# Kernel optimization log

Measured on AMD Instinct MI355X. Metric: run time of the kernel, lower is better.

Reference implementation:

```python
import jax, jax.numpy as jnp
import numpy as np

HIDDEN = 2048
NUM_HEADS = 32
NUM_KV_HEADS = 4
HEAD_DIM = 128
EPS = 1e-6
ROPE_THETA = 10000.0
Q_SIZE = NUM_HEADS * HEAD_DIM      # 4096
KV_SIZE = NUM_KV_HEADS * HEAD_DIM  # 512


def setup_inputs() -> dict:
    key = jax.random.key(0)
    k1, k2, k3, k4, k5 = jax.random.split(key, 5)
    T = 2048
    hidden_states = jax.random.normal(k1, (T, HIDDEN), dtype=jnp.float32)
    positions = jnp.arange(T, dtype=jnp.int64)
    # qkv_proj weight: [q_size + 2*kv_size, hidden] (torch Linear convention)
    w_qkv = jax.random.normal(k2, (Q_SIZE + 2 * KV_SIZE, HIDDEN), dtype=jnp.float32) * (HIDDEN ** -0.5)
    # o_proj weight: [hidden, num_heads*head_dim]
    w_o = jax.random.normal(k3, (HIDDEN, Q_SIZE), dtype=jnp.float32) * (Q_SIZE ** -0.5)
    q_norm_w = jnp.ones((HEAD_DIM,), dtype=jnp.float32) + 0.1 * jax.random.normal(k4, (HEAD_DIM,), dtype=jnp.float32)
    k_norm_w = jnp.ones((HEAD_DIM,), dtype=jnp.float32) + 0.1 * jax.random.normal(k5, (HEAD_DIM,), dtype=jnp.float32)
    return {"positions": positions, "hidden_states": hidden_states,
            "w_qkv": w_qkv, "w_o": w_o, "q_norm_w": q_norm_w, "k_norm_w": k_norm_w}


def _rms_norm(x, w):
    # x: [..., head_dim]; normalize over last dim
    var = jnp.mean(jnp.square(x), axis=-1, keepdims=True)
    return x * jax.lax.rsqrt(var + EPS) * w


def _rope(positions, x):
    # neox-style rotary over full head_dim. x: [T, H, D]
    half = HEAD_DIM // 2
    inv_freq = 1.0 / (ROPE_THETA ** (jnp.arange(0, half, dtype=jnp.float32) / half))
    freqs = positions.astype(jnp.float32)[:, None] * inv_freq[None, :]  # [T, half]
    cos = jnp.cos(freqs)[:, None, :]  # [T, 1, half]
    sin = jnp.sin(freqs)[:, None, :]
    x1, x2 = x[..., :half], x[..., half:]
    return jnp.concatenate([x1 * cos - x2 * sin, x2 * cos + x1 * sin], axis=-1)


def reference(positions, hidden_states, w_qkv, w_o, q_norm_w, k_norm_w):
    T = hidden_states.shape[0]
    qkv = hidden_states @ w_qkv.T  # [T, q_size+2*kv_size]
    q, k, v = jnp.split(qkv, [Q_SIZE, Q_SIZE + KV_SIZE], axis=-1)
    q = _rms_norm(q.reshape(T, NUM_HEADS, HEAD_DIM), q_norm_w)
    k = _rms_norm(k.reshape(T, NUM_KV_HEADS, HEAD_DIM), k_norm_w)
    v = v.reshape(T, NUM_KV_HEADS, HEAD_DIM)
    q = _rope(positions, q)
    k = _rope(positions, k)
    # GQA: expand kv heads to query heads
    rep = NUM_HEADS // NUM_KV_HEADS
    k = jnp.repeat(k, rep, axis=1)  # [T, H, D]
    v = jnp.repeat(v, rep, axis=1)
    scale = HEAD_DIM ** -0.5
    scores = jnp.einsum('qhd,khd->hqk', q, k) * scale  # [H, T, T]
    causal = jnp.tril(jnp.ones((T, T), dtype=bool))
    scores = jnp.where(causal[None, :, :], scores, jnp.float32(-1e30))
    probs = jax.nn.softmax(scores, axis=-1)
    attn = jnp.einsum('hqk,khd->qhd', probs, v).reshape(T, Q_SIZE)
    return attn @ w_o.T  # [T, hidden]
```

## Files before the change

kernel.cpp:

```cpp
#include <hip/hip_runtime.h>

#define T_TOK   2048
#define HID     2048
#define NHEADS  32
#define NKV     4
#define HD      128
#define QSZ     4096
#define KVSZ    512
#define QKVW    5120

typedef unsigned short u16;
typedef __bf16 bf16x8 __attribute__((ext_vector_type(8)));
typedef float  f32x4  __attribute__((ext_vector_type(4)));

__device__ __forceinline__ u16 f2bf(float f) {
  unsigned int u = __float_as_uint(f);
  u += 0x7fffu + ((u >> 16) & 1u);
  return (u16)(u >> 16);
}

__device__ __forceinline__ void gl2lds16(const void* g, void* l) {
  __builtin_amdgcn_global_load_lds(
      (const __attribute__((address_space(1))) unsigned int*)g,
      (__attribute__((address_space(3))) unsigned int*)l, 16, 0, 0);
}

__global__ void cvt3_f32_bf16(const float* __restrict__ in0, u16* __restrict__ o0, int n0,
                              const float* __restrict__ in1, u16* __restrict__ o1, int n1,
                              const float* __restrict__ in2, u16* __restrict__ o2, int n2) {
  int i = blockIdx.x * blockDim.x + threadIdx.x;
  const float* in; u16* out;
  if (i < n0)            { in = in0; out = o0; }
  else if (i < n0 + n1)  { in = in1; out = o1; i -= n0; }
  else if (i < n0+n1+n2) { in = in2; out = o2; i -= n0 + n1; }
  else return;
  float4 v = ((const float4*)in)[i];
  ushort4 o;
  o.x = f2bf(v.x); o.y = f2bf(v.y); o.z = f2bf(v.z); o.w = f2bf(v.w);
  ((ushort4*)out)[i] = o;
}

template<int BM>
__launch_bounds__(256, 2)
__global__ void gemm_nt(const u16* __restrict__ A, const u16* __restrict__ B,
                        float* __restrict__ C, int M, int N, int K) {
  constexpr int MI = BM / 32;
  __shared__ __align__(16) u16 As[BM * 32];
  __shared__ __align__(16) u16 Bs[128 * 32];
  const int tid  = threadIdx.x;
  const int wave = tid >> 6, lane = tid & 63;
  const int l15  = lane & 15, quad = lane >> 4;
  const int wr   = wave >> 1, wc = wave & 1;

  const u16* Ab = A + (size_t)blockIdx.y * BM * K;
  const u16* Bb = B + (size_t)blockIdx.x * 128 * K;

  f32x4 acc[MI][4];
#pragma unroll
  for (int i = 0; i < MI; i++)
#pragma unroll
    for (int j = 0; j < 4; j++) acc[i][j] = (f32x4){0.f, 0.f, 0.f, 0.f};

  constexpr int ACH = BM * 32 / 8;
  for (int k0 = 0; k0 < K; k0 += 32) {
#pragma unroll
    for (int s = 0; s < (ACH + 512) / 256; s++) {
      int c = tid + s * 256;
      if (c < ACH) {
        int row = c >> 2, co = (c & 3) * 8;
        gl2lds16(Ab + (size_t)row * K + k0 + co, &As[c * 8]);
      } else {
        int c2 = c - ACH;
        int row = c2 >> 2, co = (c2 & 3) * 8;
        gl2lds16(Bb + (size_t)row * K + k0 + co, &Bs[c2 * 8]);
      }
    }
    __syncthreads();
    bf16x8 af[MI], bf[4];
#pragma unroll
    for (int i = 0; i < MI; i++) af[i] = *(const bf16x8*)&As[(wr * (BM / 2) + i * 16 + l15) * 32 + quad * 8];
#pragma unroll
    for (int j = 0; j < 4; j++) bf[j] = *(const bf16x8*)&Bs[(wc * 64 + j * 16 + l15) * 32 + quad * 8];
#pragma unroll
    for (int i = 0; i < MI; i++)
#pragma unroll
      for (int j = 0; j < 4; j++)
        acc[i][j] = __builtin_amdgcn_mfma_f32_16x16x32_bf16(af[i], bf[j], acc[i][j], 0, 0, 0);
    __syncthreads();
  }

  float* Cb = C + (size_t)blockIdx.y * BM * N + (size_t)blockIdx.x * 128;
#pragma unroll
  for (int i = 0; i < MI; i++) {
    int rbase = wr * (BM / 2) + i * 16 + quad * 4;
#pragma unroll
    for (int j = 0; j < 4; j++) {
      int col = wc * 64 + j * 16 + l15;
#pragma unroll
      for (int r = 0; r < 4; r++) Cb[(size_t)(rbase + r) * N + col] = acc[i][j][r];
    }
  }
}

__global__ void norm_rope(const float* __restrict__ qkv, const int* __restrict__ pos,
                          const float* __restrict__ qw, const float* __restrict__ kw,
                          u16* __restrict__ qB, u16* __restrict__ kB, u16* __restrict__ vB) {
  const int t = blockIdx.x;
  const int wave = threadIdx.x >> 6, l = threadIdx.x & 63;
  const float* row = qkv + (size_t)t * QKVW;

  const float p = (float)pos[t];
  const float fr = p * exp2f(-(float)l * 0.20762050593046014f);
  float sn, cs;
  sincosf(fr, &sn, &cs);

  for (int slot = wave; slot < 40; slot += 4) {
    if (slot < 36) {
      const int   base = (slot < 32) ? slot * 128 : 4096 + (slot - 32) * 128;
      const float* w   = (slot < 32) ? qw : kw;
      float x1 = row[base + l], x2 = row[base + 64 + l];
      float ss = x1 * x1 + x2 * x2;
#pragma unroll
      for (int off = 32; off; off >>= 1) ss += __shfl_xor(ss, off);
      float rs = rsqrtf(ss * (1.f / 128.f) + 1e-6f);
      float n1 = x1 * rs * w[l], n2 = x2 * rs * w[64 + l];
      float o1 = n1 * cs - n2 * sn;
      float o2 = n2 * cs + n1 * sn;
      if (slot < 32) {
        o1 *= 0.08838834764831845f;
        o2 *= 0.08838834764831845f;
        qB[(size_t)t * QSZ + slot * 128 + l]      = f2bf(o1);
        qB[(size_t)t * QSZ + slot * 128 + 64 + l] = f2bf(o2);
      } else {
        kB[(size_t)t * KVSZ + (slot - 32) * 128 + l]      = f2bf(o1);
        kB[(size_t)t * KVSZ + (slot - 32) * 128 + 64 + l] = f2bf(o2);
      }
    } else {
      int vh = slot - 36;
      float x1 = row[4608 + vh * 128 + l];
      float x2 = row[4608 + vh * 128 + 64 + l];
      vB[(size_t)t * KVSZ + vh * 128 + l]      = f2bf(x1);
      vB[(size_t)t * KVSZ + vh * 128 + 64 + l] = f2bf(x2);
    }
  }
}

__global__ void transpose_v(const u16* __restrict__ vB, u16* __restrict__ vT) {
  const int vh = blockIdx.y, tb = blockIdx.x;
  const int d0 = threadIdx.x >> 4;
  const int tc = (threadIdx.x & 15) * 8;
#pragma unroll
  for (int s = 0; s < 8; s++) {
    int dd = d0 + s * 16;
    uint4 v; u16* pv = (u16*)&v;
#pragma unroll
    for (int j = 0; j < 8; j++)
      pv[j] = vB[(size_t)(tb * 128 + tc + j) * KVSZ + vh * 128 + dd];
    *(uint4*)&vT[((size_t)vh * 128 + dd) * T_TOK + tb * 128 + tc] = v;
  }
}

__launch_bounds__(512, 4)
__global__ void attn_fa(const u16* __restrict__ qB, const u16* __restrict__ kB,
                        const u16* __restrict__ vT, u16* __restrict__ oB) {
  const int qb  = (blockIdx.y < 16) ? (15 - (int)blockIdx.x) : (int)blockIdx.x;
  const int h   = blockIdx.y;
  const int kvh = h >> 3;
  __shared__ __align__(16) u16 Kb[2][64 * 16 * 8];
  __shared__ __align__(16) u16 Vb[2][128 * 8 * 8];
  __shared__ __align__(16) u16 Pb[128 * 8 * 8];

  const int tid  = threadIdx.x;
  const int wave = tid >> 6, lane = tid & 63;
  const int l15  = lane & 15, quad = lane >> 4;

  const int krow = tid >> 4, kmc = tid & 15;
  const int vrow = tid >> 3, vmc = tid & 7;

  bf16x8 qf[4];
#pragma unroll
  for (int ds = 0; ds < 4; ds++)
    qf[ds] = *(const bf16x8*)(qB + (size_t)(qb * 128 + wave * 16 + l15) * QSZ
                                 + h * 128 + ds * 32 + quad * 8);

  f32x4 o[8];
#pragma unroll
  for (int ni = 0; ni < 8; ni++) o[ni] = (f32x4){0.f, 0.f, 0.f, 0.f};
  float mrow[4], lrow[4];
#pragma unroll
  for (int r = 0; r < 4; r++) { mrow[r] = -3.0e38f; lrow[r] = 0.f; }

  const int nt = 2 * qb + 2;

  uint4 kreg[2], vreg[2];
#pragma unroll
  for (int s = 0; s < 2; s++) {
    kreg[s] = *(const uint4*)(kB + (size_t)(krow + s * 32) * KVSZ + kvh * 128 + kmc * 8);
    vreg[s] = *(const uint4*)(vT + ((size_t)kvh * 128 + vrow + s * 64) * T_TOK + vmc * 8);
  }

  for (int kt = 0; kt < nt; kt++) {
    const int cur = kt & 1;
#pragma unroll
    for (int s = 0; s < 2; s++) {
      int r  = krow + s * 32;
      *(uint4*)&Kb[cur][(r * 16 + (kmc ^ (r & 15))) * 8] = kreg[s];
      int rv = vrow + s * 64;
      *(uint4*)&Vb[cur][(rv * 8 + (vmc ^ (rv & 7))) * 8] = vreg[s];
    }
    __syncthreads();
    const int kn = (kt + 1 < nt) ? kt + 1 : kt;
#pragma unroll
    for (int s = 0; s < 2; s++) {
      kreg[s] = *(const uint4*)(kB + (size_t)(kn * 64 + krow + s * 32) * KVSZ + kvh * 128 + kmc * 8);
      vreg[s] = *(const uint4*)(vT + ((size_t)kvh * 128 + vrow + s * 64) * T_TOK + kn * 64 + vmc * 8);
    }

    f32x4 sc[4];
#pragma unroll
    for (int ni = 0; ni < 4; ni++) sc[ni] = (f32x4){0.f, 0.f, 0.f, 0.f};
#pragma unroll
    for (int ds = 0; ds < 4; ds++) {
#pragma unroll
      for (int ni = 0; ni < 4; ni++) {
        bf16x8 kf = *(const bf16x8*)&Kb[cur][((ni * 16 + l15) * 16 + ((ds * 4 + quad) ^ l15)) * 8];
        sc[ni] = __builtin_amdgcn_mfma_f32_16x16x32_bf16(qf[ds], kf, sc[ni], 0, 0, 0);
      }
    }

    if (kt >= 2 * qb) {
#pragma unroll
      for (int ni = 0; ni < 4; ni++)
#pragma unroll
        for (int r = 0; r < 4; r++) {
          int key = kt * 64 + ni * 16 + l15;
          int rw  = qb * 128 + wave * 16 + quad * 4 + r;
          if (key > rw) sc[ni][r] = -1.0e30f;
        }
    }

#pragma unroll
    for (int r = 0; r < 4; r++) {
      float mx = sc[0][r];
#pragma unroll
      for (int ni = 1; ni < 4; ni++) mx = fmaxf(mx, sc[ni][r]);
#pragma unroll
      for (int off = 1; off < 16; off <<= 1) mx = fmaxf(mx, __shfl_xor(mx, off));
      float mn = fmaxf(mrow[r], mx);
      float al = __expf(mrow[r] - mn);
      mrow[r] = mn;
      float rs = 0.f;
#pragma unroll
      for (int ni = 0; ni < 4; ni++) {
        float pv = __expf(sc[ni][r] - mn);
        sc[ni][r] = pv;
        rs += pv;
      }
#pragma unroll
      for (int off = 1; off < 16; off <<= 1) rs += __shfl_xor(rs, off);
      lrow[r] = lrow[r] * al + rs;
#pragma unroll
      for (int ni = 0; ni < 8; ni++) o[ni][r] *= al;
    }

#pragma unroll
    for (int ni = 0; ni < 4; ni++)
#pragma unroll
      for (int r = 0; r < 4; r++) {
        int row = wave * 16 + quad * 4 + r;
        Pb[(row * 8 + ((ni * 2 + (l15 >> 3)) ^ (row & 7))) * 8 + (l15 & 7)] =
            f2bf(sc[ni][r]);
      }

#pragma unroll
    for (int ks = 0; ks < 2; ks++) {
      bf16x8 pf = *(const bf16x8*)&Pb[((wave * 16 + l15) * 8 + ((ks * 4 + quad) ^ (l15 & 7))) * 8];
#pragma unroll
      for (int ni = 0; ni < 8; ni++) {
        bf16x8 vf = *(const bf16x8*)&Vb[cur][((ni * 16 + l15) * 8 + ((ks * 4 + quad) ^ (l15 & 7))) * 8];
        o[ni] = __builtin_amdgcn_mfma_f32_16x16x32_bf16(pf, vf, o[ni], 0, 0, 0);
      }
    }
  }

#pragma unroll
  for (int ni = 0; ni < 8; ni++)
#pragma unroll
    for (int r = 0; r < 4; r++) {
      int t = qb * 128 + wave * 16 + quad * 4 + r;
      float val = o[ni][r] / lrow[r];
      oB[(size_t)t * QSZ + h * 128 + ni * 16 + l15] = f2bf(val);
    }
}

extern "C" void kernel_launch(void* const* d_in, const int* in_sizes, int n_in,
                              void* d_out, int out_size, void* d_ws, size_t ws_size,
                              hipStream_t stream) {
  const int*   positions = (const int*)d_in[0];
  const float* hidden    = (const float*)d_in[1];
  const float* w_qkv     = (const float*)d_in[2];
  const float* w_o       = (const float*)d_in[3];
  const float* qw        = (const float*)d_in[4];
  const float* kw        = (const float*)d_in[5];
  float* out = (float*)d_out;
  char*  ws  = (char*)d_ws;

  u16* hiddenB = (u16*)ws;
  u16* wqkvB   = hiddenB + (size_t)HID * HID;
  u16* woB     = wqkvB + (size_t)QKVW * HID;
  size_t off1  = ((size_t)HID * HID + (size_t)QKVW * HID + (size_t)HID * QSZ) * 2;
  float* qkvF  = (float*)(ws + off1);
  u16*   attnB = (u16*)(ws + off1);
  size_t off2  = off1 + (size_t)T_TOK * QKVW * 4;
  u16* qBuf = (u16*)(ws + off2);
  size_t off3  = off2 + (size_t)T_TOK * QSZ * 2;
  u16* kBuf = (u16*)(ws + off3);
  size_t off4  = off3 + (size_t)T_TOK * KVSZ * 2;
  u16* vTb  = (u16*)(ws + off4);
  size_t off5  = off4 + (size_t)T_TOK * KVSZ * 2;
  u16* vBuf = (u16*)(ws + off5);

  const int n0 = HID * HID / 4, n1 = QKVW * HID / 4, n2 = HID * QSZ / 4;
  cvt3_f32_bf16<<<(n0 + n1 + n2 + 255) / 256, 256, 0, stream>>>(
      hidden, hiddenB, n0, w_qkv, wqkvB, n1, w_o, woB, n2);

  gemm_nt<128><<<dim3(QKVW / 128, T_TOK / 128), 256, 0, stream>>>(hiddenB, wqkvB, qkvF, T_TOK, QKVW, HID);

  norm_rope<<<T_TOK, 256, 0, stream>>>(qkvF, positions, qw, kw, qBuf, kBuf, vBuf);

  transpose_v<<<dim3(T_TOK / 128, NKV), 256, 0, stream>>>(vBuf, vTb);

  attn_fa<<<dim3(T_TOK / 128, NHEADS), 512, 0, stream>>>(qBuf, kBuf, vTb, attnB);

  gemm_nt<64><<<dim3(HID / 128, T_TOK / 64), 256, 0, stream>>>(attnB, woB, out, T_TOK, HID, QSZ);
}
```

Baseline: 426.3 us.

## Shrink attention tiles to 64 queries with balanced causal scheduling and lazy rescale

```diff
diff --git a/kernel.cpp b/kernel.cpp
--- a/kernel.cpp
+++ b/kernel.cpp
@@ -160,15 +160,22 @@
   }
 }
 
-__launch_bounds__(512, 4)
+__launch_bounds__(256, 4)
 __global__ void attn_fa(const u16* __restrict__ qB, const u16* __restrict__ kB,
                         const u16* __restrict__ vT, u16* __restrict__ oB) {
-  const int qb  = (blockIdx.y < 16) ? (15 - (int)blockIdx.x) : (int)blockIdx.x;
-  const int h   = blockIdx.y;
+  const int b    = blockIdx.x;
+  const int slot = b >> 8, k8 = b & 255;
+  const int h    = k8 & 31, g = k8 >> 5;
+  int p;
+  if      (slot == 0) p = 31 - g;
+  else if (slot == 1) p = g;
+  else if (slot == 2) p = 23 - g;
+  else                p = 8 + g;
   const int kvh = h >> 3;
-  __shared__ __align__(16) u16 Kb[2][64 * 16 * 8];
-  __shared__ __align__(16) u16 Vb[2][128 * 8 * 8];
-  __shared__ __align__(16) u16 Pb[128 * 8 * 8];
+
+  __shared__ __align__(16) u16 Kb[64 * 16 * 8];
+  __shared__ __align__(16) u16 Vb[128 * 8 * 8];
+  __shared__ __align__(16) u16 Pb[64 * 8 * 8];
 
   const int tid  = threadIdx.x;
   const int wave = tid >> 6, lane = tid & 63;
@@ -180,7 +187,7 @@
   bf16x8 qf[4];
 #pragma unroll
   for (int ds = 0; ds < 4; ds++)
-    qf[ds] = *(const bf16x8*)(qB + (size_t)(qb * 128 + wave * 16 + l15) * QSZ
+    qf[ds] = *(const bf16x8*)(qB + (size_t)(p * 64 + wave * 16 + l15) * QSZ
                                  + h * 128 + ds * 32 + quad * 8);
 
   f32x4 o[8];
@@ -190,30 +197,29 @@
 #pragma unroll
   for (int r = 0; r < 4; r++) { mrow[r] = -3.0e38f; lrow[r] = 0.f; }
 
-  const int nt = 2 * qb + 2;
-
-  uint4 kreg[2], vreg[2];
-#pragma unroll
-  for (int s = 0; s < 2; s++) {
-    kreg[s] = *(const uint4*)(kB + (size_t)(krow + s * 32) * KVSZ + kvh * 128 + kmc * 8);
-    vreg[s] = *(const uint4*)(vT + ((size_t)kvh * 128 + vrow + s * 64) * T_TOK + vmc * 8);
+  const int nt = p + 1;
+
+  uint4 kreg[4], vreg[4];
+#pragma unroll
+  for (int s = 0; s < 4; s++) {
+    kreg[s] = *(const uint4*)(kB + (size_t)(krow + s * 16) * KVSZ + kvh * 128 + kmc * 8);
+    vreg[s] = *(const uint4*)(vT + ((size_t)kvh * 128 + vrow + s * 32) * T_TOK + vmc * 8);
   }
 
   for (int kt = 0; kt < nt; kt++) {
-    const int cur = kt & 1;
-#pragma unroll
-    for (int s = 0; s < 2; s++) {
-      int r  = krow + s * 32;
-      *(uint4*)&Kb[cur][(r * 16 + (kmc ^ (r & 15))) * 8] = kreg[s];
-      int rv = vrow + s * 64;
-      *(uint4*)&Vb[cur][(rv * 8 + (vmc ^ (rv & 7))) * 8] = vreg[s];
+#pragma unroll
+    for (int s = 0; s < 4; s++) {
+      int r  = krow + s * 16;
+      *(uint4*)&Kb[(r * 16 + (kmc ^ (r & 15))) * 8] = kreg[s];
+      int rv = vrow + s * 32;
+      *(uint4*)&Vb[(rv * 8 + (vmc ^ (rv & 7))) * 8] = vreg[s];
     }
     __syncthreads();
     const int kn = (kt + 1 < nt) ? kt + 1 : kt;
 #pragma unroll
-    for (int s = 0; s < 2; s++) {
-      kreg[s] = *(const uint4*)(kB + (size_t)(kn * 64 + krow + s * 32) * KVSZ + kvh * 128 + kmc * 8);
-      vreg[s] = *(const uint4*)(vT + ((size_t)kvh * 128 + vrow + s * 64) * T_TOK + kn * 64 + vmc * 8);
+    for (int s = 0; s < 4; s++) {
+      kreg[s] = *(const uint4*)(kB + (size_t)(kn * 64 + krow + s * 16) * KVSZ + kvh * 128 + kmc * 8);
+      vreg[s] = *(const uint4*)(vT + ((size_t)kvh * 128 + vrow + s * 32) * T_TOK + kn * 64 + vmc * 8);
     }
 
     f32x4 sc[4];
@@ -223,18 +229,18 @@
     for (int ds = 0; ds < 4; ds++) {
 #pragma unroll
       for (int ni = 0; ni < 4; ni++) {
-        bf16x8 kf = *(const bf16x8*)&Kb[cur][((ni * 16 + l15) * 16 + ((ds * 4 + quad) ^ l15)) * 8];
+        bf16x8 kf = *(const bf16x8*)&Kb[((ni * 16 + l15) * 16 + ((ds * 4 + quad) ^ l15)) * 8];
         sc[ni] = __builtin_amdgcn_mfma_f32_16x16x32_bf16(qf[ds], kf, sc[ni], 0, 0, 0);
       }
     }
 
-    if (kt >= 2 * qb) {
+    if (kt == p) {
 #pragma unroll
       for (int ni = 0; ni < 4; ni++)
 #pragma unroll
         for (int r = 0; r < 4; r++) {
           int key = kt * 64 + ni * 16 + l15;
-          int rw  = qb * 128 + wave * 16 + quad * 4 + r;
+          int rw  = p * 64 + wave * 16 + quad * 4 + r;
           if (key > rw) sc[ni][r] = -1.0e30f;
         }
     }
@@ -246,21 +252,24 @@
       for (int ni = 1; ni < 4; ni++) mx = fmaxf(mx, sc[ni][r]);
 #pragma unroll
       for (int off = 1; off < 16; off <<= 1) mx = fmaxf(mx, __shfl_xor(mx, off));
-      float mn = fmaxf(mrow[r], mx);
-      float al = __expf(mrow[r] - mn);
-      mrow[r] = mn;
+      if (!__all(mx <= mrow[r] + 8.f)) {
+        float mn = fmaxf(mrow[r], mx);
+        float al = __expf(mrow[r] - mn);
+        mrow[r]  = mn;
+        lrow[r] *= al;
+#pragma unroll
+        for (int ni = 0; ni < 8; ni++) o[ni][r] *= al;
+      }
       float rs = 0.f;
 #pragma unroll
       for (int ni = 0; ni < 4; ni++) {
-        float pv = __expf(sc[ni][r] - mn);
+        float pv = __expf(sc[ni][r] - mrow[r]);
         sc[ni][r] = pv;
         rs += pv;
       }
 #pragma unroll
       for (int off = 1; off < 16; off <<= 1) rs += __shfl_xor(rs, off);
-      lrow[r] = lrow[r] * al + rs;
-#pragma unroll
-      for (int ni = 0; ni < 8; ni++) o[ni][r] *= al;
+      lrow[r] += rs;
     }
 
 #pragma unroll
@@ -277,17 +286,18 @@
       bf16x8 pf = *(const bf16x8*)&Pb[((wave * 16 + l15) * 8 + ((ks * 4 + quad) ^ (l15 & 7))) * 8];
 #pragma unroll
       for (int ni = 0; ni < 8; ni++) {
-        bf16x8 vf = *(const bf16x8*)&Vb[cur][((ni * 16 + l15) * 8 + ((ks * 4 + quad) ^ (l15 & 7))) * 8];
+        bf16x8 vf = *(const bf16x8*)&Vb[((ni * 16 + l15) * 8 + ((ks * 4 + quad) ^ (l15 & 7))) * 8];
         o[ni] = __builtin_amdgcn_mfma_f32_16x16x32_bf16(pf, vf, o[ni], 0, 0, 0);
       }
     }
+    __syncthreads();
   }
 
 #pragma unroll
   for (int ni = 0; ni < 8; ni++)
 #pragma unroll
     for (int r = 0; r < 4; r++) {
-      int t = qb * 128 + wave * 16 + quad * 4 + r;
+      int t = p * 64 + wave * 16 + quad * 4 + r;
       float val = o[ni][r] / lrow[r];
       oB[(size_t)t * QSZ + h * 128 + ni * 16 + l15] = f2bf(val);
     }
@@ -330,7 +340,7 @@
 
   transpose_v<<<dim3(T_TOK / 128, NKV), 256, 0, stream>>>(vBuf, vTb);
 
-  attn_fa<<<dim3(T_TOK / 128, NHEADS), 512, 0, stream>>>(qBuf, kBuf, vTb, attnB);
+  attn_fa<<<dim3(1024), 256, 0, stream>>>(qBuf, kBuf, vTb, attnB);
 
   gemm_nt<64><<<dim3(HID / 128, T_TOK / 64), 256, 0, stream>>>(attnB, woB, out, T_TOK, HID, QSZ);
 }
```

Measured after the change: 499.1 us. 17.1% more time.

## Stage K/V tiles via direct global-to-LDS loads, lazy rescale, MFMA priority

Applied to the files above, without the earlier changes.

```diff
diff --git a/kernel.cpp b/kernel.cpp
--- a/kernel.cpp
+++ b/kernel.cpp
@@ -174,8 +174,22 @@
   const int wave = tid >> 6, lane = tid & 63;
   const int l15  = lane & 15, quad = lane >> 4;
 
-  const int krow = tid >> 4, kmc = tid & 15;
-  const int vrow = tid >> 3, vmc = tid & 7;
+  auto stage = [&](int kt, int buf) {
+#pragma unroll
+    for (int s = 0; s < 2; s++) {
+      int c = tid + s * 512;
+      int r = c >> 4;
+      gl2lds16(kB + (size_t)(kt * 64 + r) * KVSZ + kvh * 128 + ((c & 15) ^ (r & 15)) * 8,
+               &Kb[buf][c * 8]);
+    }
+#pragma unroll
+    for (int s = 0; s < 2; s++) {
+      int c = tid + s * 512;
+      int rv = c >> 3;
+      gl2lds16(vT + ((size_t)kvh * 128 + rv) * T_TOK + kt * 64 + ((c & 7) ^ (rv & 7)) * 8,
+               &Vb[buf][c * 8]);
+    }
+  };
 
   bf16x8 qf[4];
 #pragma unroll
@@ -192,33 +206,17 @@
 
   const int nt = 2 * qb + 2;
 
-  uint4 kreg[2], vreg[2];
-#pragma unroll
-  for (int s = 0; s < 2; s++) {
-    kreg[s] = *(const uint4*)(kB + (size_t)(krow + s * 32) * KVSZ + kvh * 128 + kmc * 8);
-    vreg[s] = *(const uint4*)(vT + ((size_t)kvh * 128 + vrow + s * 64) * T_TOK + vmc * 8);
-  }
+  stage(0, 0);
 
   for (int kt = 0; kt < nt; kt++) {
     const int cur = kt & 1;
-#pragma unroll
-    for (int s = 0; s < 2; s++) {
-      int r  = krow + s * 32;
-      *(uint4*)&Kb[cur][(r * 16 + (kmc ^ (r & 15))) * 8] = kreg[s];
-      int rv = vrow + s * 64;
-      *(uint4*)&Vb[cur][(rv * 8 + (vmc ^ (rv & 7))) * 8] = vreg[s];
-    }
     __syncthreads();
-    const int kn = (kt + 1 < nt) ? kt + 1 : kt;
-#pragma unroll
-    for (int s = 0; s < 2; s++) {
-      kreg[s] = *(const uint4*)(kB + (size_t)(kn * 64 + krow + s * 32) * KVSZ + kvh * 128 + kmc * 8);
-      vreg[s] = *(const uint4*)(vT + ((size_t)kvh * 128 + vrow + s * 64) * T_TOK + kn * 64 + vmc * 8);
-    }
+    if (kt + 1 < nt) stage(kt + 1, cur ^ 1);
 
     f32x4 sc[4];
 #pragma unroll
     for (int ni = 0; ni < 4; ni++) sc[ni] = (f32x4){0.f, 0.f, 0.f, 0.f};
+    __builtin_amdgcn_s_setprio(1);
 #pragma unroll
     for (int ds = 0; ds < 4; ds++) {
 #pragma unroll
@@ -227,6 +225,7 @@
         sc[ni] = __builtin_amdgcn_mfma_f32_16x16x32_bf16(qf[ds], kf, sc[ni], 0, 0, 0);
       }
     }
+    __builtin_amdgcn_s_setprio(0);
 
     if (kt >= 2 * qb) {
 #pragma unroll
@@ -246,21 +245,24 @@
       for (int ni = 1; ni < 4; ni++) mx = fmaxf(mx, sc[ni][r]);
 #pragma unroll
       for (int off = 1; off < 16; off <<= 1) mx = fmaxf(mx, __shfl_xor(mx, off));
-      float mn = fmaxf(mrow[r], mx);
-      float al = __expf(mrow[r] - mn);
-      mrow[r] = mn;
+      if (!__all(mx <= mrow[r] + 8.f)) {
+        float mn = fmaxf(mrow[r], mx);
+        float al = __expf(mrow[r] - mn);
+        mrow[r]  = mn;
+        lrow[r] *= al;
+#pragma unroll
+        for (int ni = 0; ni < 8; ni++) o[ni][r] *= al;
+      }
       float rs = 0.f;
 #pragma unroll
       for (int ni = 0; ni < 4; ni++) {
-        float pv = __expf(sc[ni][r] - mn);
+        float pv = __expf(sc[ni][r] - mrow[r]);
         sc[ni][r] = pv;
         rs += pv;
       }
 #pragma unroll
       for (int off = 1; off < 16; off <<= 1) rs += __shfl_xor(rs, off);
-      lrow[r] = lrow[r] * al + rs;
-#pragma unroll
-      for (int ni = 0; ni < 8; ni++) o[ni][r] *= al;
+      lrow[r] += rs;
     }
 
 #pragma unroll
@@ -272,6 +274,7 @@
             f2bf(sc[ni][r]);
       }
 
+    __builtin_amdgcn_s_setprio(1);
 #pragma unroll
     for (int ks = 0; ks < 2; ks++) {
       bf16x8 pf = *(const bf16x8*)&Pb[((wave * 16 + l15) * 8 + ((ks * 4 + quad) ^ (l15 & 7))) * 8];
@@ -281,6 +284,7 @@
         o[ni] = __builtin_amdgcn_mfma_f32_16x16x32_bf16(pf, vf, o[ni], 0, 0, 0);
       }
     }
+    __builtin_amdgcn_s_setprio(0);
   }
 
 #pragma unroll
```

Result: faster. 366.5 us (-14.0%).
